# Kernel tuning notes

Hardware: AMD Instinct MI355X
Metric: run time of the kernel (lower is better)

## Reference

```python
import jax, jax.numpy as jnp
import numpy as np

B, CIN, H, W = 8, 32, 64, 64  # x1/x2 each 32 ch; concat -> 64
C = 2 * CIN


def setup_inputs() -> dict:
    key = jax.random.key(0)
    ks = jax.random.split(key, 8)
    s = 0.05
    return {
        "x1": jax.random.normal(ks[0], (B, CIN, H, W), jnp.float32),
        "x2": jax.random.normal(ks[1], (B, CIN, H, W), jnp.float32),
        "Wq": jax.random.normal(ks[2], (C // 2, C), jnp.float32) * s,
        "bq": jax.random.normal(ks[3], (C // 2,), jnp.float32) * s,
        "Wk": jax.random.normal(ks[4], (C // 2, C), jnp.float32) * s,
        "bk": jax.random.normal(ks[5], (C // 2,), jnp.float32) * s,
        "Wv": jax.random.normal(ks[6], (C, C), jnp.float32) * s,
        "Wsc": jax.random.normal(ks[7], (C // 2, C), jnp.float32) * s,
        "gamma": jnp.array([0.5], jnp.float32),
    }


def reference(x1, x2, Wq, bq, Wk, bk, Wv, Wsc, gamma):
    x = jnp.concatenate([x1, x2], axis=1)  # [b, c, h, w]
    b, c, h, w = x.shape
    hw = h * w
    # 1x1 convs == per-pixel linear projections
    q = (jnp.einsum('oc,bchw->bohw', Wq, x) + bq[None, :, None, None]).reshape(b, c // 2, hw)
    q = q.transpose(0, 2, 1)  # [b, hw, c/2]
    k = (jnp.einsum('oc,bchw->bohw', Wk, x) + bk[None, :, None, None]).reshape(b, c // 2, hw)
    am = jnp.einsum('bnd,bdm->bnm', q, k)  # [b, hw, hw]
    a = jax.nn.softmax(am, axis=1)  # softmax over dim=1 (queries axis) as in the torch code
    v = jnp.einsum('oc,bchw->bohw', Wv, x).reshape(b, c, hw)  # [b, c, hw]
    # out = bmm(v, a^T): out[b,c,n] = sum_m v[b,c,m] * a[b,n,m]
    out = jnp.einsum('bcm,bnm->bcn', v, a).reshape(b, c, h, w)
    out = gamma[0] * out + x
    out = jnp.einsum('oc,bchw->bohw', Wsc, out)  # [b, c/2, h, w]
    return out
```

## Files before the change

kernel.cpp:

```cpp
#include <hip/hip_runtime.h>

typedef __attribute__((ext_vector_type(8))) __bf16 bf16x8;
typedef __attribute__((ext_vector_type(4))) float f32x4;
typedef _Float16 f16x4 __attribute__((ext_vector_type(4)));
typedef unsigned int uint32;

#define HW   4096
#define CCH  64
#define DQ   32
#define OC   32
#define LOG2E 1.4426950408889634f

#define WSV_OFF  0u
#define QB_OFF   2048u
#define KB_OFF   (QB_OFF + 524288u)
#define XS_OFF   (KB_OFF + 524288u)
#define V2_OFF   (XS_OFF + 1048576u)
#define ZP_OFF   (V2_OFF + 1048576u)
#define VZC_OFF  (ZP_OFF + 262144u)
#define OUTP_OFF (VZC_OFF + 524288u)

__device__ __forceinline__ uint32 f2bf(float x) {
    uint32 u = __builtin_bit_cast(uint32, x);
    return (u + 0x7fffu + ((u >> 16) & 1u)) >> 16;
}
__device__ __forceinline__ uint32 packbf(float a, float b) {
    return f2bf(a) | (f2bf(b) << 16);
}
__device__ __forceinline__ bf16x8 ldfrag(const unsigned short* p) {
    union { uint4 u; bf16x8 f; } t;
    t.u = *(const uint4*)p;
    return t.f;
}
__device__ __forceinline__ bf16x8 asbf(uint4 u) {
    union { uint4 u; bf16x8 f; } t;
    t.u = u;
    return t.f;
}
__device__ __forceinline__ f16x4 u2h4(uint32 a, uint32 b) {
    union { uint2 u; f16x4 f; } t;
    t.u.x = a; t.u.y = b;
    return t.f;
}
__device__ __forceinline__ f16x4 pk4(float a, float b, float c, float d) {
    union { uint2 u; f16x4 f; } t;
    t.u.x = __builtin_bit_cast(uint32, __builtin_amdgcn_cvt_pkrtz(a, b));
    t.u.y = __builtin_bit_cast(uint32, __builtin_amdgcn_cvt_pkrtz(c, d));
    return t.f;
}
__device__ __forceinline__ float fexp2(float x) {
#if __has_builtin(__builtin_amdgcn_exp2f)
    return __builtin_amdgcn_exp2f(x);
#else
    return __expf(x * 0.6931471805599453f);
#endif
}

__global__ __launch_bounds__(256) void k_wcomb(const float* __restrict__ Wsc,
                                               const float* __restrict__ Wv,
                                               float* __restrict__ Wsv) {
    int t = blockIdx.x * 256 + threadIdx.x;
    if (t < OC * CCH) {
        int o = t / CCH, ci = t % CCH;
        float s = 0.f;
        #pragma unroll
        for (int c = 0; c < CCH; ++c) s += Wsc[o * CCH + c] * Wv[c * CCH + ci];
        Wsv[t] = s;
    }
}

__global__ __launch_bounds__(256) void k_proj(
    const float* __restrict__ x1, const float* __restrict__ x2,
    const float* __restrict__ Wq, const float* __restrict__ bq,
    const float* __restrict__ Wk, const float* __restrict__ bk,
    const float* __restrict__ Wsv, const float* __restrict__ Wsc,
    unsigned short* __restrict__ qb, unsigned short* __restrict__ kb,
    float* __restrict__ v2, float* __restrict__ xs) {
    int t = threadIdx.x;
    int g = __builtin_amdgcn_readfirstlane(t >> 6);
    int l = t & 63;
    int p = blockIdx.x * 64 + l;
    int b = p >> 12, n = p & 4095;
    const float* x1b = x1 + (size_t)b * 32 * HW + n;
    const float* x2b = x2 + (size_t)b * 32 * HW + n;
    float x[CCH];
    #pragma unroll
    for (int c = 0; c < 32; ++c) x[c] = x1b[(size_t)c * HW];
    #pragma unroll
    for (int c = 0; c < 32; ++c) x[32 + c] = x2b[(size_t)c * HW];

    if (g < 2) {
        const float* W    = g ? Wk : Wq;
        const float* bias = g ? bk : bq;
        float scale = g ? 1.0f : LOG2E;
        unsigned short* dst = g ? kb : qb;
        size_t row = ((size_t)b * HW + n) * DQ;
        for (int d0 = 0; d0 < DQ; d0 += 8) {
            float r[8];
            #pragma unroll
            for (int i = 0; i < 8; ++i) {
                const float* wr = W + (d0 + i) * CCH;
                float a = bias[d0 + i];
                #pragma unroll
                for (int c = 0; c < CCH; ++c) a += wr[c] * x[c];
                r[i] = a * scale;
            }
            uint4 u;
            u.x = packbf(r[0], r[1]); u.y = packbf(r[2], r[3]);
            u.z = packbf(r[4], r[5]); u.w = packbf(r[6], r[7]);
            *(uint4*)(dst + row + d0) = u;
        }
    } else {
        const float* W = (g == 2) ? Wsv : Wsc;
        float* dst     = (g == 2) ? v2  : xs;
        for (int o = 0; o < OC; ++o) {
            const float* wr = W + o * CCH;
            float a = 0.f;
            #pragma unroll
            for (int c = 0; c < CCH; ++c) a += wr[c] * x[c];
            dst[((size_t)b * OC + o) * HW + n] = a;
        }
    }
}

__global__ __launch_bounds__(128, 4) void k_stats(
    const unsigned short* __restrict__ kb, const unsigned short* __restrict__ qb,
    float* __restrict__ zp) {
    int t = threadIdx.x;
    int w = t >> 6, l = t & 63;
    int lr = l & 15, lq = l >> 4;
    int bid = blockIdx.x;
    int b = bid & 7, nc = (bid >> 3) & 7, mg = bid >> 6;
    int m0 = mg * 256 + w * 128;

    const unsigned short* kbb = kb + (size_t)b * HW * DQ;
    bf16x8 af[8];
    #pragma unroll
    for (int f = 0; f < 8; ++f)
        af[f] = ldfrag(kbb + (size_t)(m0 + f * 16 + lr) * DQ + lq * 8);

    const unsigned short* qp = qb + ((size_t)b * HW + nc * 512 + lr) * DQ + lq * 8;

    f32x4 acc[8];
    #pragma unroll
    for (int f = 0; f < 8; ++f) acc[f] = (f32x4){0.f, 0.f, 0.f, 0.f};
    f32x4 zz = {0.f, 0.f, 0.f, 0.f};

    uint4 q0 = *(const uint4*)qp;
    uint4 q1 = *(const uint4*)(qp + 16 * DQ);
    for (int i = 0; i < 32; ++i) {
        bf16x8 qf = asbf(q0);
        q0 = q1;
        if (i + 2 < 32) q1 = *(const uint4*)(qp + (size_t)(i + 2) * 16 * DQ);
        #pragma unroll
        for (int f = 0; f < 8; ++f) {
            f32x4 s = __builtin_amdgcn_mfma_f32_16x16x32_bf16(af[f], qf, zz, 0, 0, 0);
            acc[f].x += fexp2(s.x); acc[f].y += fexp2(s.y);
            acc[f].z += fexp2(s.z); acc[f].w += fexp2(s.w);
        }
    }
    #pragma unroll
    for (int f = 0; f < 8; ++f) {
        #pragma unroll
        for (int off = 1; off < 16; off <<= 1) {
            acc[f].x += __shfl_xor(acc[f].x, off);
            acc[f].y += __shfl_xor(acc[f].y, off);
            acc[f].z += __shfl_xor(acc[f].z, off);
            acc[f].w += __shfl_xor(acc[f].w, off);
        }
    }
    if (lr == 0) {
        size_t base = (size_t)nc * 32768 + (size_t)b * HW;
        #pragma unroll
        for (int f = 0; f < 8; ++f) {
            size_t p0 = base + m0 + f * 16 + lq * 4;
            zp[p0 + 0] = acc[f].x;
            zp[p0 + 1] = acc[f].y;
            zp[p0 + 2] = acc[f].z;
            zp[p0 + 3] = acc[f].w;
        }
    }
}

__global__ __launch_bounds__(256) void k_zvz(const float* __restrict__ zp,
                                             const float* __restrict__ v2,
                                             const float* __restrict__ gamma,
                                             unsigned short* __restrict__ vzc) {
    int idx = blockIdx.x * 256 + threadIdx.x;
    int i = idx >> 1, half = idx & 1;
    float s = 0.f;
    #pragma unroll
    for (int nc = 0; nc < 8; ++nc) s += zp[nc * 32768 + i];
    float zs = gamma[0] / s;
    int b = i >> 12, m = i & 4095;
    int Mb = m >> 5, mloc = m & 31;
    int ph = mloc >> 4, lqm = (mloc >> 2) & 3, j = mloc & 3;
    int o0 = half * 16;
    const float* vsrc = v2 + ((size_t)b * OC + o0) * HW + m;
    unsigned short* dst = vzc + (size_t)b * OC * HW + (size_t)Mb * 1024
                        + o0 * 32 + lqm * 8 + ph * 4 + j;
    #pragma unroll 8
    for (int o = 0; o < 16; ++o) {
        _Float16 h = (_Float16)(vsrc[(size_t)o * HW] * zs);
        dst[o * 32] = __builtin_bit_cast(unsigned short, h);
    }
}

__device__ __forceinline__ void attn_step(
    uint4 ck0, uint4 ck1, uint4 cv0, uint4 cv1,
    const bf16x8* qf, f32x4* acc0, f32x4* acc1, f32x4 zz) {
    #pragma unroll
    for (int ph = 0; ph < 2; ++ph) {
        bf16x8 a  = asbf(ph ? ck1 : ck0);
        f16x4 va0 = ph ? u2h4(cv0.z, cv0.w) : u2h4(cv0.x, cv0.y);
        f16x4 va1 = ph ? u2h4(cv1.z, cv1.w) : u2h4(cv1.x, cv1.y);
        #pragma unroll
        for (int tt = 0; tt < 8; ++tt) {
            f32x4 s = __builtin_amdgcn_mfma_f32_16x16x32_bf16(a, qf[tt], zz, 0, 0, 0);
            f16x4 p = pk4(fexp2(s.x), fexp2(s.y), fexp2(s.z), fexp2(s.w));
            acc0[tt] = __builtin_amdgcn_mfma_f32_16x16x16f16(va0, p, acc0[tt], 0, 0, 0);
            acc1[tt] = __builtin_amdgcn_mfma_f32_16x16x16f16(va1, p, acc1[tt], 0, 0, 0);
        }
    }
}

__global__ __launch_bounds__(128, 2) void k_attn(
    const unsigned short* __restrict__ qb, const unsigned short* __restrict__ kb,
    const unsigned short* __restrict__ vzc, unsigned short* __restrict__ outp) {
    int t = threadIdx.x;
    int w = t >> 6, l = t & 63;
    int lr = l & 15, lq = l >> 4;
    int bid = blockIdx.x;
    int b = bid & 7, mc = (bid >> 3) & 7, ng = bid >> 6;
    int n0 = ng * 256 + w * 128;

    bf16x8 qf[8];
    #pragma unroll
    for (int tt = 0; tt < 8; ++tt)
        qf[tt] = ldfrag(qb + ((size_t)b * HW + n0 + tt * 16 + lr) * DQ + lq * 8);

    const unsigned short* kp = kb + ((size_t)b * HW + lr) * DQ + lq * 8;
    const unsigned short* vp = vzc + (size_t)b * OC * HW + lr * 32 + lq * 8;

    f32x4 acc0[8], acc1[8];
    #pragma unroll
    for (int tt = 0; tt < 8; ++tt) {
        acc0[tt] = (f32x4){0.f, 0.f, 0.f, 0.f};
        acc1[tt] = (f32x4){0.f, 0.f, 0.f, 0.f};
    }
    f32x4 zz = {0.f, 0.f, 0.f, 0.f};

    int mbeg = mc * 512;
    uint4 kA0 = *(const uint4*)(kp + (size_t)mbeg * DQ);
    uint4 kA1 = *(const uint4*)(kp + (size_t)(mbeg + 16) * DQ);
    uint4 vA0 = *(const uint4*)(vp + (size_t)(mbeg >> 5) * 1024);
    uint4 vA1 = *(const uint4*)(vp + (size_t)(mbeg >> 5) * 1024 + 512);
    uint4 kB0 = *(const uint4*)(kp + (size_t)(mbeg + 32) * DQ);
    uint4 kB1 = *(const uint4*)(kp + (size_t)(mbeg + 48) * DQ);
    uint4 vB0 = *(const uint4*)(vp + (size_t)((mbeg + 32) >> 5) * 1024);
    uint4 vB1 = *(const uint4*)(vp + (size_t)((mbeg + 32) >> 5) * 1024 + 512);

    for (int m0 = mbeg; m0 < mbeg + 512; m0 += 64) {
        uint4 ck0 = kA0, ck1 = kA1, cv0 = vA0, cv1 = vA1;
        if (m0 + 64 < mbeg + 512) {
            kA0 = *(const uint4*)(kp + (size_t)(m0 + 64) * DQ);
            kA1 = *(const uint4*)(kp + (size_t)(m0 + 80) * DQ);
            vA0 = *(const uint4*)(vp + (size_t)((m0 + 64) >> 5) * 1024);
            vA1 = *(const uint4*)(vp + (size_t)((m0 + 64) >> 5) * 1024 + 512);
        }
        attn_step(ck0, ck1, cv0, cv1, qf, acc0, acc1, zz);
        ck0 = kB0; ck1 = kB1; cv0 = vB0; cv1 = vB1;
        if (m0 + 96 < mbeg + 512) {
            kB0 = *(const uint4*)(kp + (size_t)(m0 + 96) * DQ);
            kB1 = *(const uint4*)(kp + (size_t)(m0 + 112) * DQ);
            vB0 = *(const uint4*)(vp + (size_t)((m0 + 96) >> 5) * 1024);
            vB1 = *(const uint4*)(vp + (size_t)((m0 + 96) >> 5) * 1024 + 512);
        }
        attn_step(ck0, ck1, cv0, cv1, qf, acc0, acc1, zz);
    }

    unsigned short* ob = outp + (size_t)(mc * 8 + b) * OC * HW;
    #pragma unroll
    for (int tt = 0; tt < 8; ++tt) {
        int n_t = n0 + tt * 16 + lr;
        #pragma unroll
        for (int r = 0; r < 4; ++r) {
            int o0 = lq * 4 + r;
            ob[(size_t)o0 * HW + n_t]        = (unsigned short)f2bf(acc0[tt][r]);
            ob[(size_t)(o0 + 16) * HW + n_t] = (unsigned short)f2bf(acc1[tt][r]);
        }
    }
}

__global__ __launch_bounds__(256) void k_red(const unsigned short* __restrict__ outp,
                                             const float* __restrict__ xs,
                                             float* __restrict__ out) {
    int i = (blockIdx.x * 256 + threadIdx.x) * 4;
    float4 r = *(const float4*)(xs + i);
    const unsigned short* op = outp + i;
    #pragma unroll
    for (int mc = 0; mc < 8; ++mc) {
        uint2 p = *(const uint2*)(op + (size_t)mc * 1048576);
        r.x += __builtin_bit_cast(float, p.x << 16);
        r.y += __builtin_bit_cast(float, p.x & 0xffff0000u);
        r.z += __builtin_bit_cast(float, p.y << 16);
        r.w += __builtin_bit_cast(float, p.y & 0xffff0000u);
    }
    *(float4*)(out + i) = r;
}

extern "C" void kernel_launch(void* const* d_in, const int* in_sizes, int n_in,
                              void* d_out, int out_size, void* d_ws, size_t ws_size,
                              hipStream_t stream) {
    const float* x1    = (const float*)d_in[0];
    const float* x2    = (const float*)d_in[1];
    const float* Wq    = (const float*)d_in[2];
    const float* bq    = (const float*)d_in[3];
    const float* Wk    = (const float*)d_in[4];
    const float* bk    = (const float*)d_in[5];
    const float* Wv    = (const float*)d_in[6];
    const float* Wsc   = (const float*)d_in[7];
    const float* gamma = (const float*)d_in[8];
    float* out = (float*)d_out;
    float* ws  = (float*)d_ws;

    float*          wsv  = ws + WSV_OFF;
    unsigned short* qbp  = (unsigned short*)(ws + QB_OFF);
    unsigned short* kbp  = (unsigned short*)(ws + KB_OFF);
    float*          xsp  = ws + XS_OFF;
    float*          v2   = ws + V2_OFF;
    float*          zpp  = ws + ZP_OFF;
    unsigned short* vzc  = (unsigned short*)(ws + VZC_OFF);
    unsigned short* outp = (unsigned short*)(ws + OUTP_OFF);

    k_wcomb<<<8, 256, 0, stream>>>(Wsc, Wv, wsv);
    k_proj<<<512, 256, 0, stream>>>(x1, x2, Wq, bq, Wk, bk, wsv, Wsc,
                                    qbp, kbp, v2, xsp);
    k_stats<<<1024, 128, 0, stream>>>(kbp, qbp, zpp);
    k_zvz<<<256, 256, 0, stream>>>(zpp, v2, gamma, vzc);
    k_attn<<<1024, 128, 0, stream>>>(qbp, kbp, vzc, outp);
    k_red<<<1024, 256, 0, stream>>>(outp, xsp, out);
}
```

Baseline: 158.9 us.

## Fuse all stages into one persistent cooperative kernel with grid syncs

Replaces the six separate launches with a single cooperative persistent kernel of 256 blocks × 256 threads, separating the stages with grid.sync(). Each block now processes two or four work units per stage, and the stats and attention tiles are remapped so each block uses four waves. The aim is to remove launch gaps between kernels. In exchange, the attention stage runs at lower occupancy: only 256 blocks, with launch bounds of 256 threads and no min-blocks hint, which may raise register pressure compared with the earlier (128,2) bounds. The original multi-kernel path is kept as a fallback if the cooperative launch fails.

```diff
diff --git a/kernel.cpp b/kernel.cpp
--- a/kernel.cpp
+++ b/kernel.cpp
@@ -1,4 +1,7 @@
 #include <hip/hip_runtime.h>
+#include <hip/hip_cooperative_groups.h>
+
+namespace cg = cooperative_groups;
 
 typedef __attribute__((ext_vector_type(8))) __bf16 bf16x8;
 typedef __attribute__((ext_vector_type(4))) float f32x4;
@@ -56,30 +59,14 @@
 #endif
 }
 
-__global__ __launch_bounds__(256) void k_wcomb(const float* __restrict__ Wsc,
-                                               const float* __restrict__ Wv,
-                                               float* __restrict__ Wsv) {
-    int t = blockIdx.x * 256 + threadIdx.x;
-    if (t < OC * CCH) {
-        int o = t / CCH, ci = t % CCH;
-        float s = 0.f;
-        #pragma unroll
-        for (int c = 0; c < CCH; ++c) s += Wsc[o * CCH + c] * Wv[c * CCH + ci];
-        Wsv[t] = s;
-    }
-}
-
-__global__ __launch_bounds__(256) void k_proj(
+__device__ __forceinline__ void proj_body(
+    int p, int g,
     const float* __restrict__ x1, const float* __restrict__ x2,
     const float* __restrict__ Wq, const float* __restrict__ bq,
     const float* __restrict__ Wk, const float* __restrict__ bk,
     const float* __restrict__ Wsv, const float* __restrict__ Wsc,
     unsigned short* __restrict__ qb, unsigned short* __restrict__ kb,
     float* __restrict__ v2, float* __restrict__ xs) {
-    int t = threadIdx.x;
-    int g = __builtin_amdgcn_readfirstlane(t >> 6);
-    int l = t & 63;
-    int p = blockIdx.x * 64 + l;
     int b = p >> 12, n = p & 4095;
     const float* x1b = x1 + (size_t)b * 32 * HW + n;
     const float* x2b = x2 + (size_t)b * 32 * HW + n;
@@ -123,15 +110,12 @@
     }
 }
 
-__global__ __launch_bounds__(128, 4) void k_stats(
+__device__ __forceinline__ void stats_body(
+    int unit, int w, int lr, int lq,
     const unsigned short* __restrict__ kb, const unsigned short* __restrict__ qb,
     float* __restrict__ zp) {
-    int t = threadIdx.x;
-    int w = t >> 6, l = t & 63;
-    int lr = l & 15, lq = l >> 4;
-    int bid = blockIdx.x;
-    int b = bid & 7, nc = (bid >> 3) & 7, mg = bid >> 6;
-    int m0 = mg * 256 + w * 128;
+    int b = unit & 7, nc = (unit >> 3) & 7, mg = unit >> 6;
+    int m0 = mg * 512 + w * 128;
 
     const unsigned short* kbb = kb + (size_t)b * HW * DQ;
     bf16x8 af[8];
@@ -182,11 +166,9 @@
     }
 }
 
-__global__ __launch_bounds__(256) void k_zvz(const float* __restrict__ zp,
-                                             const float* __restrict__ v2,
-                                             const float* __restrict__ gamma,
-                                             unsigned short* __restrict__ vzc) {
-    int idx = blockIdx.x * 256 + threadIdx.x;
+__device__ __forceinline__ void zvz_body(
+    int idx, const float* __restrict__ zp, const float* __restrict__ v2,
+    const float* __restrict__ gamma, unsigned short* __restrict__ vzc) {
     int i = idx >> 1, half = idx & 1;
     float s = 0.f;
     #pragma unroll
@@ -224,15 +206,12 @@
     }
 }
 
-__global__ __launch_bounds__(128, 2) void k_attn(
+__device__ __forceinline__ void attn_body(
+    int unit, int w, int lr, int lq,
     const unsigned short* __restrict__ qb, const unsigned short* __restrict__ kb,
     const unsigned short* __restrict__ vzc, unsigned short* __restrict__ outp) {
-    int t = threadIdx.x;
-    int w = t >> 6, l = t & 63;
-    int lr = l & 15, lq = l >> 4;
-    int bid = blockIdx.x;
-    int b = bid & 7, mc = (bid >> 3) & 7, ng = bid >> 6;
-    int n0 = ng * 256 + w * 128;
+    int b = unit & 7, mc = (unit >> 3) & 7, ng = unit >> 6;
+    int n0 = ng * 512 + w * 128;
 
     bf16x8 qf[8];
     #pragma unroll
@@ -292,10 +271,10 @@
     }
 }
 
-__global__ __launch_bounds__(256) void k_red(const unsigned short* __restrict__ outp,
-                                             const float* __restrict__ xs,
-                                             float* __restrict__ out) {
-    int i = (blockIdx.x * 256 + threadIdx.x) * 4;
+__device__ __forceinline__ void red_body(
+    int idx, const unsigned short* __restrict__ outp,
+    const float* __restrict__ xs, float* __restrict__ out) {
+    int i = idx * 4;
     float4 r = *(const float4*)(xs + i);
     const unsigned short* op = outp + i;
     #pragma unroll
@@ -307,6 +286,122 @@
         r.w += __builtin_bit_cast(float, p.y & 0xffff0000u);
     }
     *(float4*)(out + i) = r;
+}
+
+__global__ __launch_bounds__(256) void k_all(
+    const float* __restrict__ x1, const float* __restrict__ x2,
+    const float* __restrict__ Wq, const float* __restrict__ bq,
+    const float* __restrict__ Wk, const float* __restrict__ bk,
+    const float* __restrict__ Wv, const float* __restrict__ Wsc,
+    const float* __restrict__ gamma, float* __restrict__ out,
+    float* __restrict__ ws) {
+    cg::grid_group grid = cg::this_grid();
+    int bid = blockIdx.x;
+    int t = threadIdx.x;
+    int w = t >> 6, l = t & 63;
+    int lr = l & 15, lq = l >> 4;
+
+    float*          wsv  = ws + WSV_OFF;
+    unsigned short* qb   = (unsigned short*)(ws + QB_OFF);
+    unsigned short* kb   = (unsigned short*)(ws + KB_OFF);
+    float*          xs   = ws + XS_OFF;
+    float*          v2   = ws + V2_OFF;
+    float*          zp   = ws + ZP_OFF;
+    unsigned short* vzc  = (unsigned short*)(ws + VZC_OFF);
+    unsigned short* outp = (unsigned short*)(ws + OUTP_OFF);
+
+    if (bid < 8) {
+        int e = bid * 256 + t;
+        int o = e >> 6, ci = e & 63;
+        float s = 0.f;
+        #pragma unroll
+        for (int c = 0; c < CCH; ++c) s += Wsc[o * CCH + c] * Wv[c * CCH + ci];
+        wsv[e] = s;
+    }
+    grid.sync();
+
+    {
+        int g = __builtin_amdgcn_readfirstlane(w);
+        for (int rep = 0; rep < 2; ++rep)
+            proj_body((bid * 2 + rep) * 64 + l, g, x1, x2, Wq, bq, Wk, bk,
+                      wsv, Wsc, qb, kb, v2, xs);
+    }
+    grid.sync();
+
+    for (int rep = 0; rep < 2; ++rep)
+        stats_body(bid * 2 + rep, w, lr, lq, kb, qb, zp);
+    grid.sync();
+
+    zvz_body(bid * 256 + t, zp, v2, gamma, vzc);
+    grid.sync();
+
+    for (int rep = 0; rep < 2; ++rep)
+        attn_body(bid * 2 + rep, w, lr, lq, qb, kb, vzc, outp);
+    grid.sync();
+
+    for (int rep = 0; rep < 4; ++rep)
+        red_body(bid * 256 + t + rep * 65536, outp, xs, out);
+}
+
+__global__ __launch_bounds__(256) void k_wcomb(const float* __restrict__ Wsc,
+                                               const float* __restrict__ Wv,
+                                               float* __restrict__ Wsv) {
+    int t = blockIdx.x * 256 + threadIdx.x;
+    if (t < OC * CCH) {
+        int o = t / CCH, ci = t % CCH;
+        float s = 0.f;
+        #pragma unroll
+        for (int c = 0; c < CCH; ++c) s += Wsc[o * CCH + c] * Wv[c * CCH + ci];
+        Wsv[t] = s;
+    }
+}
+
+__global__ __launch_bounds__(256) void k_proj(
+    const float* __restrict__ x1, const float* __restrict__ x2,
+    const float* __restrict__ Wq, const float* __restrict__ bq,
+    const float* __restrict__ Wk, const float* __restrict__ bk,
+    const float* __restrict__ Wsv, const float* __restrict__ Wsc,
+    unsigned short* __restrict__ qb, unsigned short* __restrict__ kb,
+    float* __restrict__ v2, float* __restrict__ xs) {
+    int t = threadIdx.x;
+    int g = __builtin_amdgcn_readfirstlane(t >> 6);
+    proj_body(blockIdx.x * 64 + (t & 63), g, x1, x2, Wq, bq, Wk, bk,
+              Wsv, Wsc, qb, kb, v2, xs);
+}
+
+__global__ __launch_bounds__(128, 4) void k_stats(
+    const unsigned short* __restrict__ kb, const unsigned short* __restrict__ qb,
+    float* __restrict__ zp) {
+    int t = threadIdx.x;
+    int l = t & 63;
+    int bid = blockIdx.x;
+    int unit = (bid & 63) | ((bid >> 7) << 6);
+    int w = ((bid >> 6) & 1) * 2 + (t >> 6);
+    stats_body(unit, w, l & 15, l >> 4, kb, qb, zp);
+}
+
+__global__ __launch_bounds__(256) void k_zvz(const float* __restrict__ zp,
+                                             const float* __restrict__ v2,
+                                             const float* __restrict__ gamma,
+                                             unsigned short* __restrict__ vzc) {
+    zvz_body(blockIdx.x * 256 + threadIdx.x, zp, v2, gamma, vzc);
+}
+
+__global__ __launch_bounds__(128, 2) void k_attn(
+    const unsigned short* __restrict__ qb, const unsigned short* __restrict__ kb,
+    const unsigned short* __restrict__ vzc, unsigned short* __restrict__ outp) {
+    int t = threadIdx.x;
+    int l = t & 63;
+    int bid = blockIdx.x;
+    int unit = (bid & 63) | ((bid >> 7) << 6);
+    int w = ((bid >> 6) & 1) * 2 + (t >> 6);
+    attn_body(unit, w, l & 15, l >> 4, qb, kb, vzc, outp);
+}
+
+__global__ __launch_bounds__(256) void k_red(const unsigned short* __restrict__ outp,
+                                             const float* __restrict__ xs,
+                                             float* __restrict__ out) {
+    red_body(blockIdx.x * 256 + threadIdx.x, outp, xs, out);
 }
 
 extern "C" void kernel_launch(void* const* d_in, const int* in_sizes, int n_in,
@@ -324,20 +419,25 @@
     float* out = (float*)d_out;
     float* ws  = (float*)d_ws;
 
-    float*          wsv  = ws + WSV_OFF;
-    unsigned short* qbp  = (unsigned short*)(ws + QB_OFF);
-    unsigned short* kbp  = (unsigned short*)(ws + KB_OFF);
-    float*          xsp  = ws + XS_OFF;
-    float*          v2   = ws + V2_OFF;
-    float*          zpp  = ws + ZP_OFF;
-    unsigned short* vzc  = (unsigned short*)(ws + VZC_OFF);
-    unsigned short* outp = (unsigned short*)(ws + OUTP_OFF);
-
-    k_wcomb<<<8, 256, 0, stream>>>(Wsc, Wv, wsv);
-    k_proj<<<512, 256, 0, stream>>>(x1, x2, Wq, bq, Wk, bk, wsv, Wsc,
-                                    qbp, kbp, v2, xsp);
-    k_stats<<<1024, 128, 0, stream>>>(kbp, qbp, zpp);
-    k_zvz<<<256, 256, 0, stream>>>(zpp, v2, gamma, vzc);
-    k_attn<<<1024, 128, 0, stream>>>(qbp, kbp, vzc, outp);
-    k_red<<<1024, 256, 0, stream>>>(outp, xsp, out);
-}
+    void* args[] = {&x1, &x2, &Wq, &bq, &Wk, &bk, &Wv, &Wsc, &gamma, &out, &ws};
+    hipError_t e = hipLaunchCooperativeKernel((const void*)k_all, dim3(256),
+                                              dim3(256), args, 0, stream);
+    if (e != hipSuccess) {
+        float*          wsv  = ws + WSV_OFF;
+        unsigned short* qbp  = (unsigned short*)(ws + QB_OFF);
+        unsigned short* kbp  = (unsigned short*)(ws + KB_OFF);
+        float*          xsp  = ws + XS_OFF;
+        float*          v2   = ws + V2_OFF;
+        float*          zpp  = ws + ZP_OFF;
+        unsigned short* vzc  = (unsigned short*)(ws + VZC_OFF);
+        unsigned short* outp = (unsigned short*)(ws + OUTP_OFF);
+
+        k_wcomb<<<8, 256, 0, stream>>>(Wsc, Wv, wsv);
+        k_proj<<<512, 256, 0, stream>>>(x1, x2, Wq, bq, Wk, bk, wsv, Wsc,
+                                        qbp, kbp, v2, xsp);
+        k_stats<<<1024, 128, 0, stream>>>(kbp, qbp, zpp);
+        k_zvz<<<256, 256, 0, stream>>>(zpp, v2, gamma, vzc);
+        k_attn<<<1024, 128, 0, stream>>>(qbp, kbp, vzc, outp);
+        k_red<<<1024, 256, 0, stream>>>(outp, xsp, out);
+    }
+}
```

New measurement: 331.5 us. 109% more time.
